# Kernel tuning notes

Measured on AMD Instinct MI355X. Metric: run time of the kernel, lower is better.

## Reference

```python
import jax, jax.numpy as jnp
import numpy as np

IN_SHAPE = 8192
OUT_SHAPE = 32
BATCH = 16384


def setup_inputs() -> dict:
    key = jax.random.key(0)
    kx, kw = jax.random.split(key)
    x = jax.random.normal(kx, (BATCH, IN_SHAPE), dtype=jnp.float32)
    # matches torch init: (rand*2-1)*0.001 -> uniform(-0.001, 0.001)
    weight = jax.random.uniform(kw, (OUT_SHAPE, IN_SHAPE), dtype=jnp.float32,
                                minval=-0.001, maxval=0.001)
    return {"x": x, "weight": weight}


def _binarize(weight):
    # scale = mean(|W|), detached
    scale = jax.lax.stop_gradient(jnp.mean(jnp.abs(weight)))
    clipped = jnp.clip(weight, -1.0, 1.0)
    # STE: forward value = scale*sign(W); gradient flows through clipped W
    return jax.lax.stop_gradient(scale * jnp.sign(weight) - clipped) + clipped


def reference(x, weight):
    bw = _binarize(weight)            # [out, in]
    return x @ bw.T                   # [batch, out]
```

## Files before the change

kernel.cpp:

```cpp
#include <hip/hip_runtime.h>

#define BATCH 16384
#define KDIM  8192
#define ODIM  32
#define SK    8
#define KSLICE (KDIM / SK)
#define NWAVE 4
#define THREADS (NWAVE * 64)
#define KT    32
#define NTILE (KSLICE / KT)
#define LP    36

typedef short bf16x8 __attribute__((ext_vector_type(8)));
typedef float f32x16 __attribute__((ext_vector_type(16)));

__global__ void prep_kernel(const float* __restrict__ w,
                            unsigned short* __restrict__ bwTo,
                            float* __restrict__ partial) {
    int idx = blockIdx.x * 256 + threadIdx.x;
    float v = w[idx];
    bwTo[idx] = (v > 0.f) ? 0x3F80u : ((v < 0.f) ? 0xBF80u : 0u);

    float a = fabsf(v);
    #pragma unroll
    for (int off = 32; off; off >>= 1) a += __shfl_down(a, off, 64);
    __shared__ float red[4];
    int lane = threadIdx.x & 63, wv = threadIdx.x >> 6;
    if (lane == 0) red[wv] = a;
    __syncthreads();
    if (threadIdx.x == 0)
        partial[blockIdx.x] = (red[0] + red[1]) + (red[2] + red[3]);
}

__global__ __launch_bounds__(THREADS, 6)
void main_kernel(const float* __restrict__ x,
                 const unsigned short* __restrict__ bwTo,
                 float* __restrict__ pout) {
    __shared__ union {
        float buf[2][64][LP];
        float part[2][64][33];
    } sm;

    const int tid  = threadIdx.x;
    const int wv   = __builtin_amdgcn_readfirstlane(tid >> 6);
    const int lane = tid & 63;
    const int l31  = lane & 31;
    const int lhi  = lane >> 5;
    const int kH   = wv & 1;
    const int rH   = wv >> 1;
    const int kb   = blockIdx.x & 7;
    const int rb   = blockIdx.x >> 3;
    const size_t rowbase = (size_t)rb * 64;
    const int kbase = kb * KSLICE;

    const int sr = tid >> 3;
    const int sq = tid & 7;
    const float* __restrict__ xg0 = x + (rowbase + sr) * (size_t)KDIM + kbase + 4 * sq;
    const float* __restrict__ xg1 = xg0 + (size_t)32 * KDIM;

    const unsigned short* __restrict__ bp =
        bwTo + (size_t)l31 * KDIM + kbase + kH * 16 + lhi * 8;

    f32x16 acc;
    #pragma unroll
    for (int i = 0; i < 16; ++i) acc[i] = 0.f;

    float4 v0 = *(const float4*)xg0;
    float4 v1 = *(const float4*)xg1;
    bf16x8 bcur = *(const bf16x8*)bp;
    *(float4*)&sm.buf[0][sr][4 * sq]      = v0;
    *(float4*)&sm.buf[0][sr + 32][4 * sq] = v1;

    const int xrow = rH * 32 + l31;
    const int koff = kH * 16 + lhi * 8;

    for (int t = 0; t < NTILE; ++t) {
        float4 n0, n1;
        bf16x8 bnext;
        if (t + 1 < NTILE) {
            n0 = *(const float4*)(xg0 + (t + 1) * KT);
            n1 = *(const float4*)(xg1 + (t + 1) * KT);
            bnext = *(const bf16x8*)(bp + (t + 1) * KT);
        }

        __syncthreads();

        const float4 xa = *(const float4*)&sm.buf[t & 1][xrow][koff];
        const float4 xb = *(const float4*)&sm.buf[t & 1][xrow][koff + 4];
        const float xf[8] = {xa.x, xa.y, xa.z, xa.w, xb.x, xb.y, xb.z, xb.w};
        bf16x8 ahi, alo;
        #pragma unroll
        for (int j = 0; j < 8; ++j) {
            unsigned b = __float_as_uint(xf[j]);
            float lo = xf[j] - __uint_as_float(b & 0xFFFF0000u);
            ahi[j] = (short)(b >> 16);
            alo[j] = (short)(__float_as_uint(lo) >> 16);
        }

        acc = __builtin_amdgcn_mfma_f32_32x32x16_bf16(ahi, bcur, acc, 0, 0, 0);
        acc = __builtin_amdgcn_mfma_f32_32x32x16_bf16(alo, bcur, acc, 0, 0, 0);

        if (t + 1 < NTILE) {
            *(float4*)&sm.buf[(t + 1) & 1][sr][4 * sq]      = n0;
            *(float4*)&sm.buf[(t + 1) & 1][sr + 32][4 * sq] = n1;
            bcur = bnext;
        }
    }

    __syncthreads();
    #pragma unroll
    for (int r = 0; r < 16; ++r) {
        int row32 = (r & 3) + 8 * (r >> 2) + 4 * lhi;
        sm.part[kH][rH * 32 + row32][l31] = acc[r];
    }
    __syncthreads();

    float* __restrict__ pb = pout + ((size_t)kb * BATCH + rowbase) * ODIM;
    #pragma unroll
    for (int i = 0; i < 8; ++i) {
        int j = tid + THREADS * i;
        int r = j >> 5, o = j & 31;
        pb[j] = sm.part[0][r][o] + sm.part[1][r][o];
    }
}

__global__ void reduce_kernel(const float* __restrict__ pout,
                              const float* __restrict__ partial,
                              float* __restrict__ out) {
    const int t = threadIdx.x;
    float a = (partial[t] + partial[t + 256]) + (partial[t + 512] + partial[t + 768]);
    #pragma unroll
    for (int off = 32; off; off >>= 1) a += __shfl_down(a, off, 64);
    __shared__ float red[4];
    __shared__ float sbc;
    if ((t & 63) == 0) red[t >> 6] = a;
    __syncthreads();
    if (t == 0)
        sbc = ((red[0] + red[1]) + (red[2] + red[3])) / (float)(ODIM * KDIM);
    __syncthreads();
    const float s = sbc;

    const int STRIDE = BATCH * ODIM / 4;
    int i = blockIdx.x * 256 + t;
    const float4* p = (const float4*)pout;
    float4 r = p[i];
    #pragma unroll
    for (int k = 1; k < SK; ++k) {
        float4 A = p[i + k * STRIDE];
        r.x += A.x; r.y += A.y; r.z += A.z; r.w += A.w;
    }
    r.x *= s; r.y *= s; r.z *= s; r.w *= s;
    ((float4*)out)[i] = r;
}

extern "C" void kernel_launch(void* const* d_in, const int* in_sizes, int n_in,
                              void* d_out, int out_size, void* d_ws, size_t ws_size,
                              hipStream_t stream) {
    const float* x = (const float*)d_in[0];
    const float* w = (const float*)d_in[1];
    float* out = (float*)d_out;

    float* wsf = (float*)d_ws;
    float* partial        = wsf;
    unsigned short* bwTo  = (unsigned short*)(wsf + 1024);
    float* pout           = wsf + 1024 + (ODIM * KDIM / 2);

    prep_kernel<<<1024, 256, 0, stream>>>(w, bwTo, partial);
    main_kernel<<<256 * SK, THREADS, 0, stream>>>(x, bwTo, pout);
    reduce_kernel<<<BATCH * ODIM / 4 / 256, 256, 0, stream>>>(pout, partial, out);
}
```

Baseline: 142.8 us.

## Stage x tiles with direct global-to-LDS loads and XOR-swizzled layout

```diff
diff --git a/kernel.cpp b/kernel.cpp
--- a/kernel.cpp
+++ b/kernel.cpp
@@ -5,14 +5,18 @@
 #define ODIM  32
 #define SK    8
 #define KSLICE (KDIM / SK)
-#define NWAVE 4
-#define THREADS (NWAVE * 64)
 #define KT    32
 #define NTILE (KSLICE / KT)
-#define LP    36
+#define THREADS 256
 
 typedef short bf16x8 __attribute__((ext_vector_type(8)));
 typedef float f32x16 __attribute__((ext_vector_type(16)));
+
+__device__ __forceinline__ void gload16(const float* g, void* l) {
+    __builtin_amdgcn_global_load_lds(
+        (const __attribute__((address_space(1))) void*)g,
+        (__attribute__((address_space(3))) void*)l, 16, 0, 0);
+}
 
 __global__ void prep_kernel(const float* __restrict__ w,
                             unsigned short* __restrict__ bwTo,
@@ -32,20 +36,19 @@
         partial[blockIdx.x] = (red[0] + red[1]) + (red[2] + red[3]);
 }
 
-__global__ __launch_bounds__(THREADS, 6)
+__global__ __launch_bounds__(THREADS, 8)
 void main_kernel(const float* __restrict__ x,
                  const unsigned short* __restrict__ bwTo,
                  float* __restrict__ pout) {
     __shared__ union {
-        float buf[2][64][LP];
+        float buf[2][64][KT];
         float part[2][64][33];
     } sm;
 
     const int tid  = threadIdx.x;
     const int wv   = __builtin_amdgcn_readfirstlane(tid >> 6);
     const int lane = tid & 63;
-    const int l31  = lane & 31;
-    const int lhi  = lane >> 5;
+    const int l31  = lane & 31, lhi = lane >> 5;
     const int kH   = wv & 1;
     const int rH   = wv >> 1;
     const int kb   = blockIdx.x & 7;
@@ -53,59 +56,63 @@
     const size_t rowbase = (size_t)rb * 64;
     const int kbase = kb * KSLICE;
 
-    const int sr = tid >> 3;
-    const int sq = tid & 7;
-    const float* __restrict__ xg0 = x + (rowbase + sr) * (size_t)KDIM + kbase + 4 * sq;
-    const float* __restrict__ xg1 = xg0 + (size_t)32 * KDIM;
+    const int srow   = lane >> 3;
+    const int schunk = (lane & 7) ^ srow;
+    const float* __restrict__ g0 =
+        x + (rowbase + 16 * wv + srow) * (size_t)KDIM + kbase + 4 * schunk;
+    const float* __restrict__ g1 = g0 + (size_t)8 * KDIM;
+    void* const d0a = &sm.buf[0][16 * wv][0];
+    void* const d0b = &sm.buf[0][16 * wv + 8][0];
+    void* const d1a = &sm.buf[1][16 * wv][0];
+    void* const d1b = &sm.buf[1][16 * wv + 8][0];
 
     const unsigned short* __restrict__ bp =
         bwTo + (size_t)l31 * KDIM + kbase + kH * 16 + lhi * 8;
+
+    const int arow  = rH * 32 + l31;
+    const int slot0 = ((kH << 2) | (lhi << 1)) ^ (arow & 7);
+    const int slot1 = slot0 ^ 1;
 
     f32x16 acc;
     #pragma unroll
     for (int i = 0; i < 16; ++i) acc[i] = 0.f;
 
-    float4 v0 = *(const float4*)xg0;
-    float4 v1 = *(const float4*)xg1;
+#define ISSUE(db, t) do {                                        \
+        if (db) { gload16(g0 + (t) * KT, d1a);                   \
+                  gload16(g1 + (t) * KT, d1b); }                 \
+        else    { gload16(g0 + (t) * KT, d0a);                   \
+                  gload16(g1 + (t) * KT, d0b); }                 \
+    } while (0)
+
+    ISSUE(0, 0);
     bf16x8 bcur = *(const bf16x8*)bp;
-    *(float4*)&sm.buf[0][sr][4 * sq]      = v0;
-    *(float4*)&sm.buf[0][sr + 32][4 * sq] = v1;
-
-    const int xrow = rH * 32 + l31;
-    const int koff = kH * 16 + lhi * 8;
 
     for (int t = 0; t < NTILE; ++t) {
-        float4 n0, n1;
-        bf16x8 bnext;
-        if (t + 1 < NTILE) {
-            n0 = *(const float4*)(xg0 + (t + 1) * KT);
-            n1 = *(const float4*)(xg1 + (t + 1) * KT);
-            bnext = *(const bf16x8*)(bp + (t + 1) * KT);
-        }
-
         __syncthreads();
 
-        const float4 xa = *(const float4*)&sm.buf[t & 1][xrow][koff];
-        const float4 xb = *(const float4*)&sm.buf[t & 1][xrow][koff + 4];
-        const float xf[8] = {xa.x, xa.y, xa.z, xa.w, xb.x, xb.y, xb.z, xb.w};
+        if (t + 1 < NTILE) ISSUE((t + 1) & 1, t + 1);
+        bf16x8 bnext;
+        if (t + 1 < NTILE) bnext = *(const bf16x8*)(bp + (t + 1) * KT);
+
+        const float4 xa = *(const float4*)&sm.buf[t & 1][arow][slot0 * 4];
+        const float4 xb = *(const float4*)&sm.buf[t & 1][arow][slot1 * 4];
         bf16x8 ahi, alo;
-        #pragma unroll
-        for (int j = 0; j < 8; ++j) {
-            unsigned b = __float_as_uint(xf[j]);
-            float lo = xf[j] - __uint_as_float(b & 0xFFFF0000u);
-            ahi[j] = (short)(b >> 16);
-            alo[j] = (short)(__float_as_uint(lo) >> 16);
+        {
+            const float xf[8] = {xa.x, xa.y, xa.z, xa.w, xb.x, xb.y, xb.z, xb.w};
+            #pragma unroll
+            for (int j = 0; j < 8; ++j) {
+                unsigned bu = __float_as_uint(xf[j]);
+                float lo = xf[j] - __uint_as_float(bu & 0xFFFF0000u);
+                ahi[j] = (short)(bu >> 16);
+                alo[j] = (short)(__float_as_uint(lo) >> 16);
+            }
         }
 
         acc = __builtin_amdgcn_mfma_f32_32x32x16_bf16(ahi, bcur, acc, 0, 0, 0);
         acc = __builtin_amdgcn_mfma_f32_32x32x16_bf16(alo, bcur, acc, 0, 0, 0);
-
-        if (t + 1 < NTILE) {
-            *(float4*)&sm.buf[(t + 1) & 1][sr][4 * sq]      = n0;
-            *(float4*)&sm.buf[(t + 1) & 1][sr + 32][4 * sq] = n1;
-            bcur = bnext;
-        }
+        bcur = bnext;
     }
+#undef ISSUE
 
     __syncthreads();
     #pragma unroll
@@ -161,9 +168,9 @@
     float* out = (float*)d_out;
 
     float* wsf = (float*)d_ws;
-    float* partial        = wsf;
-    unsigned short* bwTo  = (unsigned short*)(wsf + 1024);
-    float* pout           = wsf + 1024 + (ODIM * KDIM / 2);
+    float* partial       = wsf;
+    unsigned short* bwTo = (unsigned short*)(wsf + 1024);
+    float* pout          = wsf + 1024 + (ODIM * KDIM / 2);
 
     prep_kernel<<<1024, 256, 0, stream>>>(w, bwTo, partial);
     main_kernel<<<256 * SK, THREADS, 0, stream>>>(x, bwTo, pout);
```

Result: no change. 142.1 us (-0.6%).
